# Kernel optimization log

Measured on AMD Instinct MI355X. Metric: run time of the kernel, lower is better.

The kernel has to match this reference:

```python
import jax, jax.numpy as jnp
import numpy as np

NEG = -1e30  # stand-in for -inf that keeps logaddexp grad-safe


def _ctc_neg_log_likelihood(predictions, labels):
    # predictions: [B, T, C] logits; labels: [B, L] int, -1 = padding.
    # tf.nn.ctc_loss(blank_index=-1) => blank class is C-1.
    B, T, C = predictions.shape
    L = labels.shape[1]
    S = 2 * L + 1
    blank = C - 1

    label_len = jnp.sum((labels != -1).astype(jnp.int32), axis=-1)  # [B]
    labels_c = jnp.where(labels < 0, 0, labels).astype(jnp.int32)

    # Extended label sequence: blank, l1, blank, l2, ..., blank  -> [B, S]
    ext = jnp.full((B, S), blank, dtype=jnp.int32)
    ext = ext.at[:, 1::2].set(labels_c)

    # s-2 transition allowed only at label positions (odd s) with ext[s] != ext[s-2]
    same = jnp.concatenate([jnp.zeros((B, 2), bool), ext[:, 2:] == ext[:, :-2]], axis=1)
    is_label_pos = (jnp.arange(S) % 2 == 1)[None, :]
    allow2 = is_label_pos & ~same  # [B, S]

    # valid extended positions per example: s < 2*label_len + 1
    valid = jnp.arange(S)[None, :] < (2 * label_len + 1)[:, None]  # [B, S]

    log_probs = jax.nn.log_softmax(predictions, axis=-1)  # [B, T, C]
    # emission log-prob for each extended-label slot: [B, T, S]
    lp_ext = jnp.take_along_axis(log_probs, jnp.broadcast_to(ext[:, None, :], (B, T, S)), axis=2)

    has_lab = label_len > 0
    alpha0 = jnp.full((B, S), NEG, dtype=log_probs.dtype)
    alpha0 = alpha0.at[:, 0].set(lp_ext[:, 0, 0])
    alpha0 = alpha0.at[:, 1].set(jnp.where(has_lab, lp_ext[:, 0, 1], NEG))
    alpha0 = jnp.where(valid, alpha0, NEG)

    def step(alpha, lp_t):
        a1 = alpha
        a2 = jnp.pad(alpha, ((0, 0), (1, 0)), constant_values=NEG)[:, :S]
        a3 = jnp.pad(alpha, ((0, 0), (2, 0)), constant_values=NEG)[:, :S]
        a3 = jnp.where(allow2, a3, NEG)
        new = jnp.logaddexp(jnp.logaddexp(a1, a2), a3) + lp_t
        new = jnp.where(valid, new, NEG)
        return new, None

    lp_rest = jnp.moveaxis(lp_ext[:, 1:], 1, 0)  # [T-1, B, S]
    alphaT, _ = jax.lax.scan(step, alpha0, lp_rest)

    idx1 = (2 * label_len)[:, None]              # final blank
    idx2 = jnp.maximum(idx1 - 1, 0)              # final label
    a_end1 = jnp.take_along_axis(alphaT, idx1, axis=1)[:, 0]
    a_end2 = jnp.take_along_axis(alphaT, idx2, axis=1)[:, 0]
    a_end2 = jnp.where(has_lab, a_end2, NEG)
    log_lik = jnp.logaddexp(a_end1, a_end2)
    return -log_lik  # [B]


def setup_inputs() -> dict:
    key = jax.random.key(0)
    k1, k2 = jax.random.split(key)
    B, T, C, L = 1024, 384, 96, 48
    labels = jax.random.randint(k1, (B, L), 0, C - 1).astype(jnp.int64)
    predictions = jax.random.normal(k2, (B, T, C), dtype=jnp.float32)
    return {"labels": labels, "predictions": predictions}


def reference(labels, predictions):
    per_example = _ctc_neg_log_likelihood(predictions, labels)
    return jnp.mean(per_example)
```

## Files before the change

### kernel.cpp

```cpp
#include <hip/hip_runtime.h>

constexpr int Tt = 384;
constexpr int Cc = 96;
constexpr int Ll = 48;
constexpr int Gg = 8;
constexpr int NG = 24;

#define L2E 1.4426950408889634f
#define LN2 0.6931471805599453f
#define LNEG (-3.0e38f)

template <int CTRL, int RM = 0xF>
__device__ __forceinline__ float dppf(float x) {
    return __int_as_float(
        __builtin_amdgcn_update_dpp(0, __float_as_int(x), CTRL, RM, 0xF, true));
}
template <int CTRL>
__device__ __forceinline__ int dppi(int x) {
    return __builtin_amdgcn_update_dpp(0, x, CTRL, 0xF, 0xF, true);
}
__device__ __forceinline__ float bcast63(float x) {
    return __int_as_float(__builtin_amdgcn_readlane(__float_as_int(x), 63));
}
__device__ __forceinline__ float wsum(float x) {
    x += dppf<0x111>(x);
    x += dppf<0x112>(x);
    x += dppf<0x114>(x);
    x += dppf<0x118>(x);
    x += dppf<0x142, 0xA>(x);
    x += dppf<0x143, 0xC>(x);
    return bcast63(x);
}
__device__ __forceinline__ float shup1(float x) { return dppf<0x138>(x); }
__device__ __forceinline__ float shdn1(float x) { return dppf<0x130>(x); }
__device__ __forceinline__ float exp2i(int d) {
    d = d < -126 ? -126 : (d > 126 ? 126 : d);
    return __int_as_float((d + 127) << 23);
}

template <bool FWD>
__device__ __forceinline__ void prod_load(const float2* __restrict__ rp2, float2* q,
                                          int g, int lane) {
#pragma unroll
    for (int j = 0; j < Gg; ++j) {
        int k = g * Gg + j;
        int t = FWD ? k : (Tt - 1 - k);
        q[j] = (lane < 48) ? rp2[(size_t)t * 48 + lane] : make_float2(-1e4f, -1e4f);
    }
}

__device__ __forceinline__ void softmax_group(const float2* q, float* pl, float* pb,
                                              int idx_h, int bitsel) {
#pragma unroll
    for (int j = 0; j < Gg; ++j) {
        float ex = __builtin_amdgcn_exp2f(q[j].x * L2E);
        float ey = __builtin_amdgcn_exp2f(q[j].y * L2E);
        float gb = __shfl(ey, 47, 64);
        float g0 = __shfl(ex, idx_h, 64);
        float g1 = __shfl(ey, idx_h, 64);
        float s  = wsum(ex + ey);
        float rZ = __builtin_amdgcn_rcpf(s);
        pl[j] = (bitsel ? g1 : g0) * rZ;
        pb[j] = gb * rZ;
    }
}

template <bool FWD>
__device__ __forceinline__ void dp_group(const float* pl, const float* pb,
                                         float allow2f, float& st_e, float& st_o,
                                         int& ls, float& f, float& a2f) {
#pragma unroll
    for (int j = 0; j < Gg; ++j) {
        if (FWD) {
            float sh = shup1(st_o);
            float t0 = st_e + st_o;
            float ne = fmaf(f, sh, st_e) * pb[j];
            float no = fmaf(a2f, sh, t0) * pl[j];
            st_e = ne; st_o = no;
        } else {
            float en = shdn1(st_e);
            float on = shdn1(st_o);
            float ne = (st_e + st_o) * pb[j];
            float no = fmaf(a2f, on, fmaf(f, en, st_o)) * pl[j];
            st_e = ne; st_o = no;
        }
    }
    float m = fmaxf(st_e, st_o);
    bool z  = (m == 0.0f);
    int eb  = (__float_as_int(m) >> 23) & 0xFF;
    eb = eb > 253 ? 253 : eb;
    float r = z ? 1.0f : __int_as_float((254 - eb) << 23);
    st_e *= r; st_o *= r;
    ls += z ? 0 : (eb - 127);
#pragma unroll
    for (int it = 0; it < 8; ++it) {
        int lsn = FWD ? dppi<0x138>(ls) : dppi<0x130>(ls);
        ls = z ? lsn : ls;
    }
    int lsn2 = FWD ? dppi<0x138>(ls) : dppi<0x130>(ls);
    f   = exp2i(lsn2 - ls);
    a2f = allow2f * f;
}

template <bool FWD>
__device__ __forceinline__ void run_half(const float2* __restrict__ rp2, int lane,
                                         int idx_h, int bitsel, float allow2f,
                                         float& st_e, float& st_o, int& ls,
                                         float& f, float& a2f) {
    float2 q0[Gg], q1[Gg];
    float plA[Gg], pbA[Gg], plB[Gg], pbB[Gg];
    prod_load<FWD>(rp2, q0, 0, lane);
    prod_load<FWD>(rp2, q1, 1, lane);
    softmax_group(q0, plA, pbA, idx_h, bitsel);
    for (int g2 = 0; g2 < NG / 2; ++g2) {
        bool more = (g2 < NG / 2 - 1);
        if (more) prod_load<FWD>(rp2, q0, 2 * g2 + 2, lane);
        softmax_group(q1, plB, pbB, idx_h, bitsel);
        dp_group<FWD>(plA, pbA, allow2f, st_e, st_o, ls, f, a2f);
        if (more) prod_load<FWD>(rp2, q1, 2 * g2 + 3, lane);
        if (more) softmax_group(q0, plA, pbA, idx_h, bitsel);
        dp_group<FWD>(plB, pbB, allow2f, st_e, st_o, ls, f, a2f);
    }
}

__global__ __launch_bounds__(128) void ctc_fb(const int* __restrict__ labels,
                                              const float* __restrict__ pred,
                                              float* __restrict__ nll) {
    const int b    = blockIdx.x;
    const int lane = threadIdx.x & 63;
    const int wv   = threadIdx.x >> 6;
    const float2* rp2 = (const float2*)(pred + (size_t)b * Tt * Cc);

    __shared__ float sbe[64], sbo[64];
    __shared__ int   slsb[64];

    int v = (lane < Ll) ? labels[(size_t)b * Ll + lane] : -1;
    int present = (lane < Ll) && (v != -1);
    int labv = (v < 0) ? 0 : v;
    unsigned long long pm = __ballot(present);
    int len = __popcll(pm);
    int idx_h  = labv >> 1;
    int bitsel = labv & 1;
    int lab_p = __shfl(labv, (lane - 1) & 63, 64);
    int lab_n = __shfl(labv, (lane + 1) & 63, 64);

    float st_e, st_o = 0.0f, f = 1.0f, a2f, allow2f;
    int   ls = 0;

    if (wv == 0) {
        allow2f = (lane >= 1 && labv != lab_p) ? 1.0f : 0.0f;
        st_e = (lane == 0) ? 1.0f : 0.0f;
        a2f = allow2f;
        run_half<true>(rp2, lane, idx_h, bitsel, allow2f, st_e, st_o, ls, f, a2f);
    } else {
        allow2f = (labv != lab_n) ? 1.0f : 0.0f;
        st_e = (lane == len) ? 1.0f : 0.0f;
        a2f = allow2f;
        run_half<false>(rp2, lane, idx_h, bitsel, allow2f, st_e, st_o, ls, f, a2f);
        sbe[lane]  = st_e;
        sbo[lane]  = st_o;
        slsb[lane] = ls;
    }
    __syncthreads();

    if (wv == 0) {
        float sh  = shup1(st_o);
        int   lsu = dppi<0x138>(ls);
        float fup = exp2i(lsu - ls);
        float Ae = fmaf(fup, sh, st_e);
        float Ao = fmaf(allow2f * fup, sh, st_e + st_o);
        float be = sbe[lane], bo = sbo[lane];
        float base = (float)(ls + slsb[lane]);
        float l1 = (Ae > 0.0f && be > 0.0f) ? __log2f(Ae) + __log2f(be) + base : LNEG;
        float l2 = (Ao > 0.0f && bo > 0.0f) ? __log2f(Ao) + __log2f(bo) + base : LNEG;
        float mm = fmaxf(l1, l2);
#pragma unroll
        for (int off = 32; off >= 1; off >>= 1) mm = fmaxf(mm, __shfl_xor(mm, off, 64));
        float ss = exp2f(l1 - mm) + exp2f(l2 - mm);
#pragma unroll
        for (int off = 32; off >= 1; off >>= 1) ss += __shfl_xor(ss, off, 64);
        if (lane == 0) {
            float ll = (mm + __log2f(ss)) * LN2;
            nll[b] = -ll;
        }
    }
}

__global__ __launch_bounds__(256) void ctc_mean(const float* __restrict__ nll,
                                                float* __restrict__ out, float invB) {
    __shared__ double part[256];
    double s = 0.0;
#pragma unroll
    for (int i = 0; i < 4; ++i) s += (double)nll[threadIdx.x + 256 * i];
    part[threadIdx.x] = s;
    __syncthreads();
#pragma unroll
    for (int w = 128; w >= 1; w >>= 1) {
        if (threadIdx.x < w) part[threadIdx.x] += part[threadIdx.x + w];
        __syncthreads();
    }
    if (threadIdx.x == 0) out[0] = (float)(part[0] * (double)invB);
}

extern "C" void kernel_launch(void* const* d_in, const int* in_sizes, int n_in,
                              void* d_out, int out_size, void* d_ws, size_t ws_size,
                              hipStream_t stream) {
    const int*   labels = (const int*)d_in[0];
    const float* pred   = (const float*)d_in[1];
    float*       out    = (float*)d_out;
    float*       nll    = (float*)d_ws;

    const int B = in_sizes[0] / Ll;

    hipLaunchKernelGGL(ctc_fb, dim3(B), dim3(128), 0, stream, labels, pred, nll);
    hipLaunchKernelGGL(ctc_mean, dim3(1), dim3(256), 0, stream, nll, out, 1.0f / (float)B);
}
```

Baseline: 221.6 us.

## Split softmax producers from DP consumers via shared-memory ring buffer

Each block grows from 2 to 8 waves. Six producer waves, three per direction, load logits and compute the softmax emission probabilities for interleaved time groups. They write these into a shared-memory ring buffer guarded by flags. The two DP waves spin on the flags and run only the forward/backward recurrence, which takes the softmax work off the serial critical path. The cost is spin-wait synchronisation overhead, heavy LDS use per block that limits occupancy, and more waves competing for issue slots.

```diff
diff --git a/kernel.cpp b/kernel.cpp
--- a/kernel.cpp
+++ b/kernel.cpp
@@ -5,6 +5,9 @@
 constexpr int Ll = 48;
 constexpr int Gg = 8;
 constexpr int NG = 24;
+constexpr int RSo = 50;
+constexpr int SLOT = Gg * RSo;
+constexpr int RING = 12;
 
 #define L2E 1.4426950408889634f
 #define LN2 0.6931471805599453f
@@ -38,13 +41,12 @@
     return __int_as_float((d + 127) << 23);
 }
 
-template <bool FWD>
-__device__ __forceinline__ void prod_load(const float2* __restrict__ rp2, float2* q,
-                                          int g, int lane) {
+__device__ __forceinline__ void load_group(const float2* __restrict__ rp2, float2* q,
+                                           int dir, int g, int lane) {
 #pragma unroll
     for (int j = 0; j < Gg; ++j) {
         int k = g * Gg + j;
-        int t = FWD ? k : (Tt - 1 - k);
+        int t = dir ? (Tt - 1 - k) : k;
         q[j] = (lane < 48) ? rp2[(size_t)t * 48 + lane] : make_float2(-1e4f, -1e4f);
     }
 }
@@ -66,22 +68,28 @@
 }
 
 template <bool FWD>
-__device__ __forceinline__ void dp_group(const float* pl, const float* pb,
+__device__ __forceinline__ void dp_group(const float* __restrict__ pr, int lane,
                                          float allow2f, float& st_e, float& st_o,
                                          int& ls, float& f, float& a2f) {
+    float plC[Gg], pbC[Gg];
+#pragma unroll
+    for (int j = 0; j < Gg; ++j) {
+        plC[j] = pr[j * RSo + lane];
+        pbC[j] = pr[j * RSo + 49];
+    }
 #pragma unroll
     for (int j = 0; j < Gg; ++j) {
         if (FWD) {
             float sh = shup1(st_o);
             float t0 = st_e + st_o;
-            float ne = fmaf(f, sh, st_e) * pb[j];
-            float no = fmaf(a2f, sh, t0) * pl[j];
+            float ne = fmaf(f, sh, st_e) * pbC[j];
+            float no = fmaf(a2f, sh, t0) * plC[j];
             st_e = ne; st_o = no;
         } else {
             float en = shdn1(st_e);
             float on = shdn1(st_o);
-            float ne = (st_e + st_o) * pb[j];
-            float no = fmaf(a2f, on, fmaf(f, en, st_o)) * pl[j];
+            float ne = (st_e + st_o) * pbC[j];
+            float no = fmaf(a2f, on, fmaf(f, en, st_o)) * plC[j];
             st_e = ne; st_o = no;
         }
     }
@@ -102,37 +110,24 @@
     a2f = allow2f * f;
 }
 
-template <bool FWD>
-__device__ __forceinline__ void run_half(const float2* __restrict__ rp2, int lane,
-                                         int idx_h, int bitsel, float allow2f,
-                                         float& st_e, float& st_o, int& ls,
-                                         float& f, float& a2f) {
-    float2 q0[Gg], q1[Gg];
-    float plA[Gg], pbA[Gg], plB[Gg], pbB[Gg];
-    prod_load<FWD>(rp2, q0, 0, lane);
-    prod_load<FWD>(rp2, q1, 1, lane);
-    softmax_group(q0, plA, pbA, idx_h, bitsel);
-    for (int g2 = 0; g2 < NG / 2; ++g2) {
-        bool more = (g2 < NG / 2 - 1);
-        if (more) prod_load<FWD>(rp2, q0, 2 * g2 + 2, lane);
-        softmax_group(q1, plB, pbB, idx_h, bitsel);
-        dp_group<FWD>(plA, pbA, allow2f, st_e, st_o, ls, f, a2f);
-        if (more) prod_load<FWD>(rp2, q1, 2 * g2 + 3, lane);
-        if (more) softmax_group(q0, plA, pbA, idx_h, bitsel);
-        dp_group<FWD>(plB, pbB, allow2f, st_e, st_o, ls, f, a2f);
-    }
-}
-
-__global__ __launch_bounds__(128) void ctc_fb(const int* __restrict__ labels,
-                                              const float* __restrict__ pred,
-                                              float* __restrict__ nll) {
+__global__ __launch_bounds__(512, 8) void ctc_fb(const int* __restrict__ labels,
+                                                 const float* __restrict__ pred,
+                                                 float* __restrict__ nll) {
     const int b    = blockIdx.x;
     const int lane = threadIdx.x & 63;
     const int wv   = threadIdx.x >> 6;
     const float2* rp2 = (const float2*)(pred + (size_t)b * Tt * Cc);
 
+    __shared__ float plb[2 * RING * SLOT + 16];
+    __shared__ int   flg[2 * NG];
+    __shared__ int   cons[2];
     __shared__ float sbe[64], sbo[64];
     __shared__ int   slsb[64];
+
+    for (int i = threadIdx.x; i < 2 * RING * SLOT + 16; i += 512) plb[i] = 0.0f;
+    if (threadIdx.x < 2 * NG) flg[threadIdx.x] = 0;
+    if (threadIdx.x < 2) cons[threadIdx.x] = 0;
+    __syncthreads();
 
     int v = (lane < Ll) ? labels[(size_t)b * Ll + lane] : -1;
     int present = (lane < Ll) && (v != -1);
@@ -144,46 +139,84 @@
     int lab_p = __shfl(labv, (lane - 1) & 63, 64);
     int lab_n = __shfl(labv, (lane + 1) & 63, 64);
 
-    float st_e, st_o = 0.0f, f = 1.0f, a2f, allow2f;
-    int   ls = 0;
-
-    if (wv == 0) {
-        allow2f = (lane >= 1 && labv != lab_p) ? 1.0f : 0.0f;
-        st_e = (lane == 0) ? 1.0f : 0.0f;
+    if (wv >= 2) {
+        const int dir = (wv >= 5) ? 1 : 0;
+        const int q   = wv - (dir ? 5 : 2);
+        float2 qa[Gg], qb[Gg];
+        load_group(rp2, qa, dir, q, lane);
+        if (q + 3 < NG) load_group(rp2, qb, dir, q + 3, lane);
+#pragma unroll
+        for (int i = 0; i < 8; ++i) {
+            const int g = q + 3 * i;
+            float pl[Gg], pb[Gg];
+            softmax_group((i & 1) ? qb : qa, pl, pb, idx_h, bitsel);
+            if (i + 2 < 8) load_group(rp2, (i & 1) ? qb : qa, dir, q + 3 * (i + 2), lane);
+            if (g >= RING) {
+                while (*(volatile int*)&cons[dir] < g - RING + 1)
+                    __builtin_amdgcn_s_sleep(1);
+            }
+            float* dst = &plb[(dir * RING + (g % RING)) * SLOT];
+#pragma unroll
+            for (int j = 0; j < Gg; ++j)
+                if (lane < RSo) dst[j * RSo + lane] = (lane == 49) ? pb[j] : pl[j];
+            asm volatile("s_waitcnt lgkmcnt(0)" ::: "memory");
+            if (lane == 0) *(volatile int*)&flg[dir * NG + g] = 1;
+        }
+    } else {
+        const int dir = wv;
+        float st_e, st_o = 0.0f, f = 1.0f, a2f, allow2f;
+        int   ls = 0;
+        if (dir == 0) {
+            allow2f = (lane >= 1 && labv != lab_p) ? 1.0f : 0.0f;
+            st_e = (lane == 0) ? 1.0f : 0.0f;
+        } else {
+            allow2f = (labv != lab_n) ? 1.0f : 0.0f;
+            st_e = (lane == len) ? 1.0f : 0.0f;
+        }
         a2f = allow2f;
-        run_half<true>(rp2, lane, idx_h, bitsel, allow2f, st_e, st_o, ls, f, a2f);
-    } else {
-        allow2f = (labv != lab_n) ? 1.0f : 0.0f;
-        st_e = (lane == len) ? 1.0f : 0.0f;
-        a2f = allow2f;
-        run_half<false>(rp2, lane, idx_h, bitsel, allow2f, st_e, st_o, ls, f, a2f);
-        sbe[lane]  = st_e;
-        sbo[lane]  = st_o;
-        slsb[lane] = ls;
+        for (int g = 0; g < NG; ++g) {
+            while (!*(volatile int*)&flg[dir * NG + g]) __builtin_amdgcn_s_sleep(1);
+            asm volatile("" ::: "memory");
+            const float* pr = &plb[(dir * RING + (g % RING)) * SLOT];
+            if (dir == 0)
+                dp_group<true>(pr, lane, allow2f, st_e, st_o, ls, f, a2f);
+            else
+                dp_group<false>(pr, lane, allow2f, st_e, st_o, ls, f, a2f);
+            asm volatile("" ::: "memory");
+            if (lane == 0) *(volatile int*)&cons[dir] = g + 1;
+        }
+        if (dir == 1) {
+            sbe[lane]  = st_e;
+            sbo[lane]  = st_o;
+            slsb[lane] = ls;
+        }
+        if (dir == 0) {
+        }
+        if (dir == 0) {
+            __syncthreads();
+            float sh  = shup1(st_o);
+            int   lsu = dppi<0x138>(ls);
+            float fup = exp2i(lsu - ls);
+            float Ae = fmaf(fup, sh, st_e);
+            float Ao = fmaf(allow2f * fup, sh, st_e + st_o);
+            float be = sbe[lane], bo = sbo[lane];
+            float base = (float)(ls + slsb[lane]);
+            float l1 = (Ae > 0.0f && be > 0.0f) ? __log2f(Ae) + __log2f(be) + base : LNEG;
+            float l2 = (Ao > 0.0f && bo > 0.0f) ? __log2f(Ao) + __log2f(bo) + base : LNEG;
+            float mm = fmaxf(l1, l2);
+#pragma unroll
+            for (int off = 32; off >= 1; off >>= 1) mm = fmaxf(mm, __shfl_xor(mm, off, 64));
+            float ss = exp2f(l1 - mm) + exp2f(l2 - mm);
+#pragma unroll
+            for (int off = 32; off >= 1; off >>= 1) ss += __shfl_xor(ss, off, 64);
+            if (lane == 0) {
+                float ll = (mm + __log2f(ss)) * LN2;
+                nll[b] = -ll;
+            }
+            return;
+        }
     }
     __syncthreads();
-
-    if (wv == 0) {
-        float sh  = shup1(st_o);
-        int   lsu = dppi<0x138>(ls);
-        float fup = exp2i(lsu - ls);
-        float Ae = fmaf(fup, sh, st_e);
-        float Ao = fmaf(allow2f * fup, sh, st_e + st_o);
-        float be = sbe[lane], bo = sbo[lane];
-        float base = (float)(ls + slsb[lane]);
-        float l1 = (Ae > 0.0f && be > 0.0f) ? __log2f(Ae) + __log2f(be) + base : LNEG;
-        float l2 = (Ao > 0.0f && bo > 0.0f) ? __log2f(Ao) + __log2f(bo) + base : LNEG;
-        float mm = fmaxf(l1, l2);
-#pragma unroll
-        for (int off = 32; off >= 1; off >>= 1) mm = fmaxf(mm, __shfl_xor(mm, off, 64));
-        float ss = exp2f(l1 - mm) + exp2f(l2 - mm);
-#pragma unroll
-        for (int off = 32; off >= 1; off >>= 1) ss += __shfl_xor(ss, off, 64);
-        if (lane == 0) {
-            float ll = (mm + __log2f(ss)) * LN2;
-            nll[b] = -ll;
-        }
-    }
 }
 
 __global__ __launch_bounds__(256) void ctc_mean(const float* __restrict__ nll,
@@ -212,6 +245,6 @@
 
     const int B = in_sizes[0] / Ll;
 
-    hipLaunchKernelGGL(ctc_fb, dim3(B), dim3(128), 0, stream, labels, pred, nll);
+    hipLaunchKernelGGL(ctc_fb, dim3(B), dim3(512), 0, stream, labels, pred, nll);
     hipLaunchKernelGGL(ctc_mean, dim3(1), dim3(256), 0, stream, nll, out, 1.0f / (float)B);
 }
```

After: 238.0 us. +7.4%, slower.
